# Optimization experiments

Measured on AMD Instinct MI355X. Metric: run time of the kernel, lower is better.

Reference implementation:

```python
import jax, jax.numpy as jnp
import numpy as np

HASHCODE_LEN = 8   # config.attention_hashcode_len (tau)
NUM_HEAD = 12      # config.num_attention_heads
KERNEL = 9         # config.attention_conv_kernel_size
B, H, S, D = 2, 12, 2048, 64


def _l2_normalize(x, eps=1e-12):
    # yoso.normalize: L2-normalize along last (head_dim) axis
    return x / jnp.maximum(jnp.linalg.norm(x, axis=-1, keepdims=True), eps)


def setup_inputs() -> dict:
    key = jax.random.key(0)
    kq, kk, kv, kw = jax.random.split(key, 4)
    Q = jax.random.normal(kq, (B, H, S, D), jnp.float32)
    K = jax.random.normal(kk, (B, H, S, D), jnp.float32)
    V = jax.random.normal(kv, (B, H, S, D), jnp.float32)
    mask = jnp.ones((B, S), jnp.float32)
    conv_w = jax.random.normal(kw, (H, 1, KERNEL, 1), jnp.float32) * 0.02
    return {"Q": Q, "K": K, "V": V, "mask": mask, "conv_w": conv_w}


def reference(Q, K, V, mask, conv_w):
    # conv skip path: depthwise (groups=num_head) Conv2d over the seq axis of masked V
    Vm = V * mask[:, None, :, None]                       # [B,H,S,D]
    conv_V = jax.lax.conv_general_dilated(
        Vm, conv_w, window_strides=(1, 1),
        padding=((KERNEL // 2, KERNEL // 2), (0, 0)),
        dimension_numbers=("NCHW", "OIHW", "NCHW"),
        feature_group_count=H)

    # yoso_e exact-expectation branch (num_hash_f < 0): normalize Q, K, then
    # attention weight = E[hash collision] = (1 - arccos(q.k)/pi)^hashcode_len
    Qn = _l2_normalize(Q)
    Kn = _l2_normalize(K)
    qk = jnp.einsum("bhsd,bhtd->bhst", Qn, Kn)            # [B,H,S,S]
    qk = jnp.clip(qk, -1.0 + 1e-6, 1.0 - 1e-6)            # keep arccos grad finite
    w = (1.0 - jnp.arccos(qk) / jnp.pi) ** HASHCODE_LEN
    w = w * mask[:, None, None, :]                        # key-side mask
    X = jnp.einsum("bhst,bhtd->bhsd", w, V)
    X = X * mask[:, None, :, None]                        # query-side mask
    X = _l2_normalize(X)                                  # yoso.normalize(X)
    return X + conv_V
```

## Files before the change

### kernel.cpp

```cpp
#include <hip/hip_runtime.h>
#include <hip/hip_bf16.h>
#include <math.h>

typedef __attribute__((ext_vector_type(4))) float f32x4;
typedef __attribute__((ext_vector_type(8))) short bf16x8;
typedef __attribute__((ext_vector_type(4))) int i32x4;

#define NB 2
#define NH 12
#define NS 2048
#define ND 64
#define NKER 9
#define BH (NB*NH)
#define BHS (NB*NH*NS)
#define NT (NS/64)

using bf16 = __hip_bfloat16;

__device__ __forceinline__ f32x4 mfma16x16x32_bf16(bf16x8 a, bf16x8 b, f32x4 c) {
  return __builtin_amdgcn_mfma_f32_16x16x32_bf16(a, b, c, 0, 0, 0);
}

__global__ void normalize_qk(const float* __restrict__ Q, const float* __restrict__ K,
                             bf16* __restrict__ Qn, bf16* __restrict__ Kn) {
  int wid  = (blockIdx.x * blockDim.x + threadIdx.x) >> 6;
  int lane = threadIdx.x & 63;
  if (wid >= 2 * BHS) return;
  const float* src; bf16* dst; int row;
  if (wid < BHS) { src = Q; dst = Qn; row = wid; }
  else           { src = K; dst = Kn; row = wid - BHS; }
  float v  = src[(size_t)row * ND + lane];
  float ss = v * v;
  #pragma unroll
  for (int m = 1; m < 64; m <<= 1) ss += __shfl_xor(ss, m);
  float scale = 1.0f / fmaxf(sqrtf(ss), 1e-12f);
  dst[(size_t)row * ND + lane] = __float2bfloat16(v * scale);
}

__global__ __launch_bounds__(256) void conv_vt(
    const float* __restrict__ V, const float* __restrict__ mask,
    const float* __restrict__ cw, float* __restrict__ out, bf16* __restrict__ Vmt) {
  __shared__ float tile[72][68];
  __shared__ float wsm[NKER];
  int bh = blockIdx.y, b = bh / NH, h = bh % NH;
  int s0 = blockIdx.x * 64;
  int tid = threadIdx.x;
  if (tid < NKER) wsm[tid] = cw[h * NKER + tid];

  int r  = tid >> 2;
  int c0 = (tid & 3) * 16;
  #pragma unroll
  for (int pass = 0; pass < 2; ++pass) {
    int rr = r + pass * 64;
    if (pass == 0 || tid < 32) {
      int gs = s0 - NKER / 2 + rr;
      bool ok = (gs >= 0 && gs < NS);
      float m = ok ? mask[b * NS + gs] : 0.f;
      #pragma unroll
      for (int j = 0; j < 16; ++j)
        tile[rr][c0 + j] = ok ? V[((size_t)bh * NS + gs) * ND + c0 + j] * m : 0.f;
    }
  }
  __syncthreads();

  {
    int s = tid >> 2;
    float acc[16];
    #pragma unroll
    for (int j = 0; j < 16; ++j) acc[j] = 0.f;
    #pragma unroll
    for (int k = 0; k < NKER; ++k) {
      float w = wsm[k];
      #pragma unroll
      for (int j = 0; j < 16; ++j) acc[j] += tile[s + k][c0 + j] * w;
    }
    float* dst = out + ((size_t)bh * NS + s0 + s) * ND + c0;
    #pragma unroll
    for (int j = 0; j < 16; ++j) dst[j] = acc[j];
  }
  {
    int d = tid >> 2;
    bf16* dst = Vmt + (size_t)bh * ND * NS + (size_t)d * NS + s0 + c0;
    #pragma unroll
    for (int j = 0; j < 16; ++j)
      dst[j] = __float2bfloat16(tile[NKER / 2 + c0 + j][d]);
  }
}

__global__ __launch_bounds__(512) void yoso_attn(
    const bf16* __restrict__ Qn, const bf16* __restrict__ Kn,
    const bf16* __restrict__ Vmt, const float* __restrict__ mask,
    float* __restrict__ out) {
  __shared__ __align__(16) char lds[48 * 1024];

  int tid  = threadIdx.x;
  int wave = tid >> 6;
  int lane = tid & 63;
  int lo   = lane & 15;
  int hi   = lane >> 4;
  int qsub = wave >> 1;
  int kh   = wave & 1;
  int bh   = blockIdx.y;
  int b    = bh / NH;
  int q0   = blockIdx.x * 64;

  const bf16* Qbh = Qn  + (size_t)bh * NS * ND;
  const bf16* Kbh = Kn  + (size_t)bh * NS * ND;
  const bf16* Vbh = Vmt + (size_t)bh * ND * NS;

  int qrow = q0 + qsub * 16 + lo;
  bf16x8 aq0 = *(const bf16x8*)(Qbh + (size_t)qrow * ND + hi * 8);
  bf16x8 aq1 = *(const bf16x8*)(Qbh + (size_t)qrow * ND + 32 + hi * 8);

  f32x4 xacc[4];
  #pragma unroll
  for (int i = 0; i < 4; ++i) xacc[i] = (f32x4){0.f, 0.f, 0.f, 0.f};

  int row0 = tid >> 3, coff0 = (tid & 7) * 16;
  int dst0 = row0 * 128 + (coff0 ^ ((row0 & 7) << 4));
  const char* Ks0 = (const char*)(Kbh + (size_t)row0 * ND) + coff0;
  const char* Vs0 = (const char*)(Vbh + (size_t)row0 * NS) + coff0;

  *(i32x4*)(lds + dst0)        = *(const i32x4*)Ks0;
  *(i32x4*)(lds + 8192 + dst0) = *(const i32x4*)Vs0;

  char* pw = lds + 32768 + wave * 2048;
  i32x4 kr, vr;

  for (int kt = 0; kt < NT; ++kt) {
    __syncthreads();
    if (kt < NT - 1) {
      kr = *(const i32x4*)(Ks0 + (size_t)(kt + 1) * 8192);
      vr = *(const i32x4*)(Vs0 + (size_t)(kt + 1) * 128);
    }
    char* kb = lds + (kt & 1) * 16384;
    char* vb = kb + 8192;

    #pragma unroll
    for (int cgl = 0; cgl < 2; ++cgl) {
      int cg   = kh * 2 + cgl;
      f32x4 s  = (f32x4){0.f, 0.f, 0.f, 0.f};
      int krow = cg * 16 + lo;
      const char* kbase = kb + krow * 128;
      int sw = (krow & 7) << 4;
      bf16x8 bk0 = *(const bf16x8*)(kbase + ((hi * 16) ^ sw));
      bf16x8 bk1 = *(const bf16x8*)(kbase + ((64 + hi * 16) ^ sw));
      s = mfma16x16x32_bf16(aq0, bk0, s);
      s = mfma16x16x32_bf16(aq1, bk1, s);
      #pragma unroll
      for (int r = 0; r < 4; ++r) {
        float x = s[r];
        float a = fminf(fabsf(x), 0.999999f);
        float sq = __builtin_amdgcn_sqrtf(1.0f - a);
        float p = fmaf(fmaf(fmaf(-0.005961377f, a, 0.02363857f), a,
                            -0.06751758f), a, 0.49998939f);
        float u = sq * p;
        float t = (x >= 0.0f) ? (1.0f - u) : u;
        float t2 = t * t, t4 = t2 * t2, w = t4 * t4;
        int prow = hi * 4 + r;
        int pcol = cgl * 16 + lo;
        *(bf16*)(pw + prow * 128 + ((pcol * 2) ^ ((prow & 7) << 4))) = __float2bfloat16(w);
      }
    }

    {
      const char* pbase = pw + lo * 128;
      bf16x8 ap = *(const bf16x8*)(pbase + ((hi * 16) ^ ((lo & 7) << 4)));
      #pragma unroll
      for (int dg = 0; dg < 4; ++dg) {
        int drow = dg * 16 + lo;
        const char* vbase = vb + drow * 128;
        bf16x8 bv = *(const bf16x8*)(vbase + ((kh * 64 + hi * 16) ^ ((drow & 7) << 4)));
        xacc[dg] = mfma16x16x32_bf16(ap, bv, xacc[dg]);
      }
    }

    if (kt < NT - 1) {
      char* kbn = lds + ((kt + 1) & 1) * 16384;
      *(i32x4*)(kbn + dst0)        = kr;
      *(i32x4*)(kbn + 8192 + dst0) = vr;
    }
  }

  __syncthreads();
  float* cmb = (float*)(lds + 32768);
  if (kh == 1) {
    #pragma unroll
    for (int r = 0; r < 4; ++r)
      #pragma unroll
      for (int dg = 0; dg < 4; ++dg)
        cmb[qsub * 1024 + (hi * 4 + r) * 64 + dg * 16 + lo] = xacc[dg][r];
  }
  __syncthreads();
  if (kh == 0) {
    #pragma unroll
    for (int r = 0; r < 4; ++r) {
      int row = q0 + qsub * 16 + hi * 4 + r;
      float m = mask[b * NS + row];
      float vals[4];
      float ss = 0.f;
      #pragma unroll
      for (int dg = 0; dg < 4; ++dg) {
        float x = (xacc[dg][r] + cmb[qsub * 1024 + (hi * 4 + r) * 64 + dg * 16 + lo]) * m;
        vals[dg] = x;
        ss += x * x;
      }
      #pragma unroll
      for (int mm = 1; mm < 16; mm <<= 1) ss += __shfl_xor(ss, mm);
      float scale = 1.0f / fmaxf(sqrtf(ss), 1e-12f);
      size_t base = ((size_t)bh * NS + row) * ND;
      #pragma unroll
      for (int dg = 0; dg < 4; ++dg)
        out[base + dg * 16 + lo] += vals[dg] * scale;
    }
  }
}

extern "C" void kernel_launch(void* const* d_in, const int* in_sizes, int n_in,
                              void* d_out, int out_size, void* d_ws, size_t ws_size,
                              hipStream_t stream) {
  const float* Q    = (const float*)d_in[0];
  const float* K    = (const float*)d_in[1];
  const float* V    = (const float*)d_in[2];
  const float* mask = (const float*)d_in[3];
  const float* cw   = (const float*)d_in[4];
  float* out = (float*)d_out;

  bf16* Qn  = (bf16*)d_ws;
  bf16* Kn  = Qn + (size_t)BHS * ND;
  bf16* Vmt = Kn + (size_t)BHS * ND;

  normalize_qk<<<2 * BHS / 4, 256, 0, stream>>>(Q, K, Qn, Kn);
  conv_vt<<<dim3(NS / 64, BH), 256, 0, stream>>>(V, mask, cw, out, Vmt);
  yoso_attn<<<dim3(NS / 64, BH), 512, 0, stream>>>(Qn, Kn, Vmt, mask, out);
}
```

Before: 93.27 us.

## Fuse Q/K normalization into prep and attention kernels, remap blocks, simplify arccos polynomial

Removes the separate normalize_qk launch. K normalization moves into the conv/transpose prep kernel, and Q is normalized in registers inside the attention kernel straight from fp32. The attention grid is flattened and remapped so that consecutive blocks cover 8 different heads. Vectorized bf16 stores with manual round-to-nearest-even replace the scalar stores. The arccos weight now uses a single-sided polynomial in (1-x), which drops the abs and sign select but relies on that polynomial staying accurate for negative dot products.

After: 88.89 us. -4.7%, faster.

```diff
diff --git a/kernel.cpp b/kernel.cpp
--- a/kernel.cpp
+++ b/kernel.cpp
@@ -2,9 +2,9 @@
 #include <hip/hip_bf16.h>
 #include <math.h>
 
-typedef __attribute__((ext_vector_type(4))) float f32x4;
-typedef __attribute__((ext_vector_type(8))) short bf16x8;
-typedef __attribute__((ext_vector_type(4))) int i32x4;
+typedef __attribute__((ext_vector_type(4)))  float f32x4;
+typedef __attribute__((ext_vector_type(8)))  short bf16x8;
+typedef __attribute__((ext_vector_type(4)))  int   i32x4;
 
 #define NB 2
 #define NH 12
@@ -17,29 +17,20 @@
 
 using bf16 = __hip_bfloat16;
 
-__device__ __forceinline__ f32x4 mfma16x16x32_bf16(bf16x8 a, bf16x8 b, f32x4 c) {
+__device__ __forceinline__ f32x4 mfma16(bf16x8 a, bf16x8 b, f32x4 c) {
   return __builtin_amdgcn_mfma_f32_16x16x32_bf16(a, b, c, 0, 0, 0);
 }
 
-__global__ void normalize_qk(const float* __restrict__ Q, const float* __restrict__ K,
-                             bf16* __restrict__ Qn, bf16* __restrict__ Kn) {
-  int wid  = (blockIdx.x * blockDim.x + threadIdx.x) >> 6;
-  int lane = threadIdx.x & 63;
-  if (wid >= 2 * BHS) return;
-  const float* src; bf16* dst; int row;
-  if (wid < BHS) { src = Q; dst = Qn; row = wid; }
-  else           { src = K; dst = Kn; row = wid - BHS; }
-  float v  = src[(size_t)row * ND + lane];
-  float ss = v * v;
-  #pragma unroll
-  for (int m = 1; m < 64; m <<= 1) ss += __shfl_xor(ss, m);
-  float scale = 1.0f / fmaxf(sqrtf(ss), 1e-12f);
-  dst[(size_t)row * ND + lane] = __float2bfloat16(v * scale);
-}
-
-__global__ __launch_bounds__(256) void conv_vt(
-    const float* __restrict__ V, const float* __restrict__ mask,
-    const float* __restrict__ cw, float* __restrict__ out, bf16* __restrict__ Vmt) {
+__device__ __forceinline__ unsigned short bf16rne(float f) {
+  unsigned u = __builtin_bit_cast(unsigned, f);
+  u += 0x7FFFu + ((u >> 16) & 1u);
+  return (unsigned short)(u >> 16);
+}
+
+__global__ __launch_bounds__(256) void prep(
+    const float* __restrict__ K, const float* __restrict__ V,
+    const float* __restrict__ mask, const float* __restrict__ cw,
+    float* __restrict__ out, bf16* __restrict__ Kn, bf16* __restrict__ Vmt) {
   __shared__ float tile[72][68];
   __shared__ float wsm[NKER];
   int bh = blockIdx.y, b = bh / NH, h = bh % NH;
@@ -49,6 +40,24 @@
 
   int r  = tid >> 2;
   int c0 = (tid & 3) * 16;
+
+  {
+    const float* Kr = K + ((size_t)bh * NS + s0 + r) * ND + c0;
+    float v[16]; float ss = 0.f;
+    #pragma unroll
+    for (int j = 0; j < 16; ++j) { v[j] = Kr[j]; ss += v[j] * v[j]; }
+    ss += __shfl_xor(ss, 1); ss += __shfl_xor(ss, 2);
+    float sc = rsqrtf(fmaxf(ss, 1e-24f));
+    bf16x8 o0, o1;
+    #pragma unroll
+    for (int j = 0; j < 8; ++j) {
+      o0[j] = (short)bf16rne(v[j] * sc);
+      o1[j] = (short)bf16rne(v[8 + j] * sc);
+    }
+    bf16* dst = Kn + ((size_t)bh * NS + s0 + r) * ND + c0;
+    *(bf16x8*)dst = o0; *(bf16x8*)(dst + 8) = o1;
+  }
+
   #pragma unroll
   for (int pass = 0; pass < 2; ++pass) {
     int rr = r + pass * 64;
@@ -64,7 +73,6 @@
   __syncthreads();
 
   {
-    int s = tid >> 2;
     float acc[16];
     #pragma unroll
     for (int j = 0; j < 16; ++j) acc[j] = 0.f;
@@ -72,23 +80,26 @@
     for (int k = 0; k < NKER; ++k) {
       float w = wsm[k];
       #pragma unroll
-      for (int j = 0; j < 16; ++j) acc[j] += tile[s + k][c0 + j] * w;
-    }
-    float* dst = out + ((size_t)bh * NS + s0 + s) * ND + c0;
+      for (int j = 0; j < 16; ++j) acc[j] += tile[r + k][c0 + j] * w;
+    }
+    float* dst = out + ((size_t)bh * NS + s0 + r) * ND + c0;
     #pragma unroll
     for (int j = 0; j < 16; ++j) dst[j] = acc[j];
   }
   {
-    int d = tid >> 2;
-    bf16* dst = Vmt + (size_t)bh * ND * NS + (size_t)d * NS + s0 + c0;
-    #pragma unroll
-    for (int j = 0; j < 16; ++j)
-      dst[j] = __float2bfloat16(tile[NKER / 2 + c0 + j][d]);
+    bf16x8 o0, o1;
+    #pragma unroll
+    for (int j = 0; j < 8; ++j) {
+      o0[j] = (short)bf16rne(tile[NKER / 2 + c0 + j][r]);
+      o1[j] = (short)bf16rne(tile[NKER / 2 + c0 + 8 + j][r]);
+    }
+    bf16* dst = Vmt + (size_t)bh * ND * NS + (size_t)r * NS + s0 + c0;
+    *(bf16x8*)dst = o0; *(bf16x8*)(dst + 8) = o1;
   }
 }
 
 __global__ __launch_bounds__(512) void yoso_attn(
-    const bf16* __restrict__ Qn, const bf16* __restrict__ Kn,
+    const float* __restrict__ Q, const bf16* __restrict__ Kn,
     const bf16* __restrict__ Vmt, const float* __restrict__ mask,
     float* __restrict__ out) {
   __shared__ __align__(16) char lds[48 * 1024];
@@ -100,38 +111,62 @@
   int hi   = lane >> 4;
   int qsub = wave >> 1;
   int kh   = wave & 1;
-  int bh   = blockIdx.y;
-  int b    = bh / NH;
-  int q0   = blockIdx.x * 64;
-
-  const bf16* Qbh = Qn  + (size_t)bh * NS * ND;
+
+  int bx  = blockIdx.x;
+  int idx = bx >> 3;
+  int bh  = (bx & 7) + 8 * (idx >> 5);
+  int qg  = idx & 31;
+  int b   = bh / NH;
+  int q0  = qg * 64;
+
   const bf16* Kbh = Kn  + (size_t)bh * NS * ND;
   const bf16* Vbh = Vmt + (size_t)bh * ND * NS;
 
-  int qrow = q0 + qsub * 16 + lo;
-  bf16x8 aq0 = *(const bf16x8*)(Qbh + (size_t)qrow * ND + hi * 8);
-  bf16x8 aq1 = *(const bf16x8*)(Qbh + (size_t)qrow * ND + 32 + hi * 8);
+  bf16x8 aq0, aq1;
+  {
+    int qrow = q0 + qsub * 16 + lo;
+    const float* Qr = Q + ((size_t)bh * NS + qrow) * ND;
+    f32x4 a0 = *(const f32x4*)(Qr + hi * 8);
+    f32x4 a1 = *(const f32x4*)(Qr + hi * 8 + 4);
+    f32x4 a2 = *(const f32x4*)(Qr + 32 + hi * 8);
+    f32x4 a3 = *(const f32x4*)(Qr + 32 + hi * 8 + 4);
+    float ss = 0.f;
+    #pragma unroll
+    for (int j = 0; j < 4; ++j)
+      ss += a0[j] * a0[j] + a1[j] * a1[j] + a2[j] * a2[j] + a3[j] * a3[j];
+    ss += __shfl_xor(ss, 16);
+    ss += __shfl_xor(ss, 32);
+    float sc = rsqrtf(fmaxf(ss, 1e-24f));
+    #pragma unroll
+    for (int j = 0; j < 4; ++j) {
+      aq0[j]     = (short)bf16rne(a0[j] * sc);
+      aq0[4 + j] = (short)bf16rne(a1[j] * sc);
+      aq1[j]     = (short)bf16rne(a2[j] * sc);
+      aq1[4 + j] = (short)bf16rne(a3[j] * sc);
+    }
+  }
 
   f32x4 xacc[4];
   #pragma unroll
   for (int i = 0; i < 4; ++i) xacc[i] = (f32x4){0.f, 0.f, 0.f, 0.f};
 
-  int row0 = tid >> 3, coff0 = (tid & 7) * 16;
-  int dst0 = row0 * 128 + (coff0 ^ ((row0 & 7) << 4));
-  const char* Ks0 = (const char*)(Kbh + (size_t)row0 * ND) + coff0;
-  const char* Vs0 = (const char*)(Vbh + (size_t)row0 * NS) + coff0;
-
-  *(i32x4*)(lds + dst0)        = *(const i32x4*)Ks0;
-  *(i32x4*)(lds + 8192 + dst0) = *(const i32x4*)Vs0;
+  int kr = tid >> 3, kc = (tid & 7) * 16;
+  int kd = kr * 128 + (kc ^ ((kr & 7) << 4));
+  int vd = 8192 + kd;
+  const char* KsA = (const char*)Kbh + (size_t)kr * 128 + kc;
+  const char* VsA = (const char*)Vbh + (size_t)kr * (NS * 2) + kc;
+
+  *(i32x4*)(lds + kd) = *(const i32x4*)KsA;
+  *(i32x4*)(lds + vd) = *(const i32x4*)VsA;
 
   char* pw = lds + 32768 + wave * 2048;
-  i32x4 kr, vr;
+  i32x4 kA, vA;
 
   for (int kt = 0; kt < NT; ++kt) {
     __syncthreads();
     if (kt < NT - 1) {
-      kr = *(const i32x4*)(Ks0 + (size_t)(kt + 1) * 8192);
-      vr = *(const i32x4*)(Vs0 + (size_t)(kt + 1) * 128);
+      kA = *(const i32x4*)(KsA + (size_t)(kt + 1) * 8192);
+      vA = *(const i32x4*)(VsA + (size_t)(kt + 1) * 128);
     }
     char* kb = lds + (kt & 1) * 16384;
     char* vb = kb + 8192;
@@ -145,21 +180,22 @@
       int sw = (krow & 7) << 4;
       bf16x8 bk0 = *(const bf16x8*)(kbase + ((hi * 16) ^ sw));
       bf16x8 bk1 = *(const bf16x8*)(kbase + ((64 + hi * 16) ^ sw));
-      s = mfma16x16x32_bf16(aq0, bk0, s);
-      s = mfma16x16x32_bf16(aq1, bk1, s);
+      s = mfma16(aq0, bk0, s);
+      s = mfma16(aq1, bk1, s);
       #pragma unroll
       for (int r = 0; r < 4; ++r) {
-        float x = s[r];
-        float a = fminf(fabsf(x), 0.999999f);
-        float sq = __builtin_amdgcn_sqrtf(1.0f - a);
-        float p = fmaf(fmaf(fmaf(-0.005961377f, a, 0.02363857f), a,
-                            -0.06751758f), a, 0.49998939f);
-        float u = sq * p;
-        float t = (x >= 0.0f) ? (1.0f - u) : u;
-        float t2 = t * t, t4 = t2 * t2, w = t4 * t4;
+        float x  = fminf(s[r], 0.999999f);
+        float u  = 1.0f - x;
+        float sq = __builtin_amdgcn_sqrtf(u);
+        float gg = fmaf(fmaf(fmaf(fmaf(8.54787e-4f, u, 2.512043e-3f), u,
+                                  8.440465e-3f), u, 3.7513178e-2f), u,
+                        0.45015816f);
+        float t1 = fmaf(-sq, gg, 1.0f);
+        float t2 = t1 * t1, t4 = t2 * t2, w = t4 * t4;
         int prow = hi * 4 + r;
         int pcol = cgl * 16 + lo;
-        *(bf16*)(pw + prow * 128 + ((pcol * 2) ^ ((prow & 7) << 4))) = __float2bfloat16(w);
+        *(short*)(pw + prow * 128 + ((pcol * 2) ^ ((prow & 7) << 4))) =
+            (short)bf16rne(w);
       }
     }
 
@@ -171,14 +207,14 @@
         int drow = dg * 16 + lo;
         const char* vbase = vb + drow * 128;
         bf16x8 bv = *(const bf16x8*)(vbase + ((kh * 64 + hi * 16) ^ ((drow & 7) << 4)));
-        xacc[dg] = mfma16x16x32_bf16(ap, bv, xacc[dg]);
+        xacc[dg] = mfma16(ap, bv, xacc[dg]);
       }
     }
 
     if (kt < NT - 1) {
-      char* kbn = lds + ((kt + 1) & 1) * 16384;
-      *(i32x4*)(kbn + dst0)        = kr;
-      *(i32x4*)(kbn + 8192 + dst0) = vr;
+      char* nb = lds + ((kt + 1) & 1) * 16384;
+      *(i32x4*)(nb + kd)        = kA;
+      *(i32x4*)(nb + 8192 + kd) = vA;
     }
   }
 
@@ -207,7 +243,7 @@
       }
       #pragma unroll
       for (int mm = 1; mm < 16; mm <<= 1) ss += __shfl_xor(ss, mm);
-      float scale = 1.0f / fmaxf(sqrtf(ss), 1e-12f);
+      float scale = rsqrtf(fmaxf(ss, 1e-24f));
       size_t base = ((size_t)bh * NS + row) * ND;
       #pragma unroll
       for (int dg = 0; dg < 4; ++dg)
@@ -226,11 +262,9 @@
   const float* cw   = (const float*)d_in[4];
   float* out = (float*)d_out;
 
-  bf16* Qn  = (bf16*)d_ws;
-  bf16* Kn  = Qn + (size_t)BHS * ND;
+  bf16* Kn  = (bf16*)d_ws;
   bf16* Vmt = Kn + (size_t)BHS * ND;
 
-  normalize_qk<<<2 * BHS / 4, 256, 0, stream>>>(Q, K, Qn, Kn);
-  conv_vt<<<dim3(NS / 64, BH), 256, 0, stream>>>(V, mask, cw, out, Vmt);
-  yoso_attn<<<dim3(NS / 64, BH), 512, 0, stream>>>(Qn, Kn, Vmt, mask, out);
-}
+  prep<<<dim3(NS / 64, BH), 256, 0, stream>>>(K, V, mask, cw, out, Kn, Vmt);
+  yoso_attn<<<(NS / 64) * BH, 512, 0, stream>>>(Q, Kn, Vmt, mask, out);
+}
```
